# Kernel tuning notes

Hardware: AMD Instinct MI355X
Metric: run time of the kernel (lower is better)

Reference implementation:

```python
import jax, jax.numpy as jnp
import numpy as np

ENT_TYPE_SIZE = 9
INNER_DIM = 64
NEG_INF = 1e12


def _rope_interleaved(x, cos_pos, sin_pos):
    # x: (B, S, H, D); rotate interleaved pairs: (x0,x1)->(x0*c - x1*s, x1*c + x0*s)
    x2 = jnp.stack([-x[..., 1::2], x[..., ::2]], axis=-1).reshape(x.shape)
    return x * cos_pos + x2 * sin_pos


def setup_inputs() -> dict:
    key = jax.random.key(0)
    k1, k2 = jax.random.split(key)
    B, S, H = 16, 512, 768
    out_dim = ENT_TYPE_SIZE * INNER_DIM * 2  # 1152
    last_hidden_state = jax.random.normal(k1, (B, S, H), dtype=jnp.float32)
    attention_mask = jnp.ones((B, S), dtype=jnp.float32)
    W_dense = jax.random.normal(k2, (H, out_dim), dtype=jnp.float32) * (1.0 / np.sqrt(H))
    b_dense = jnp.zeros((out_dim,), dtype=jnp.float32)
    return {
        "last_hidden_state": last_hidden_state,
        "attention_mask": attention_mask,
        "W_dense": W_dense,
        "b_dense": b_dense,
    }


def reference(last_hidden_state, attention_mask, W_dense, b_dense):
    B, S, H = last_hidden_state.shape
    ent, inner = ENT_TYPE_SIZE, INNER_DIM

    # dense projection then split into per-entity-type q/k vectors
    proj = last_hidden_state @ W_dense + b_dense            # (B, S, ent*2*inner)
    proj = proj.reshape(B, S, ent, 2 * inner)
    qw, kw = proj[..., :inner], proj[..., inner:]           # (B, S, ent, inner)

    # inline RoPE, interleaved sin/cos layout per sinusoidal_position_embedding
    pos = jnp.arange(S, dtype=jnp.float32)[:, None]         # (S, 1)
    idx = jnp.arange(inner // 2, dtype=jnp.float32)
    freqs = pos * jnp.power(10000.0, -2.0 * idx / inner)    # (S, inner/2)
    cos_pos = jnp.repeat(jnp.cos(freqs), 2, axis=-1)[None, :, None, :]  # (1,S,1,inner)
    sin_pos = jnp.repeat(jnp.sin(freqs), 2, axis=-1)[None, :, None, :]
    qw = _rope_interleaved(qw, cos_pos, sin_pos)
    kw = _rope_interleaved(kw, cos_pos, sin_pos)

    # pairwise span scores
    logits = jnp.einsum('bmhd,bnhd->bhmn', qw, kw)          # (B, ent, S, S)

    # padding mask on key positions (canonical GlobalPointer masking)
    pad = attention_mask[:, None, None, :]                  # (B,1,1,S)
    logits = logits * pad - (1.0 - pad) * NEG_INF

    # strict lower triangle masked out (only spans with start <= end)
    tril = jnp.tril(jnp.ones((S, S), dtype=logits.dtype), -1)
    logits = logits - tril * NEG_INF

    return logits / (inner ** 0.5)
```

## Files before the change

kernel.cpp:

```cpp
#include <hip/hip_runtime.h>
#include <hip/hip_bf16.h>
#include <cstdint>

typedef __bf16 bf8 __attribute__((ext_vector_type(8)));
typedef __bf16 bf4 __attribute__((ext_vector_type(4)));
typedef float  f4  __attribute__((ext_vector_type(4)));

typedef const void __attribute__((address_space(1)))* as1_cvp;
typedef void       __attribute__((address_space(3)))* as3_vp;

#define NEG_INF_F 1000000000000.0f

__device__ __forceinline__ void lds_load16(const __bf16* g, __bf16* l) {
    __builtin_amdgcn_global_load_lds((as1_cvp)g, (as3_vp)l, 16, 0, 0);
}

__device__ __forceinline__ void gemm_tile_core(
    const __bf16* __restrict__ Atile, const __bf16* __restrict__ Btile,
    int lda, int ldb, int Ktot,
    __bf16* sA, __bf16* sB, f4 acc[4][4])
{
    const int t    = threadIdx.x;
    const int wave = t >> 6;
    const int lane = t & 63;
    const int quad = lane >> 4;
    const int m16  = lane & 15;
    const int wm   = (wave >> 1) * 64;
    const int wn   = (wave & 1) * 64;

    for (int k0 = 0; k0 < Ktot; k0 += 32) {
        __syncthreads();
#pragma unroll
        for (int i = 0; i < 2; ++i) {
            const int f   = i * 256 + t;
            const int row = f >> 2;
            const int ch  = (f & 3) * 8;
            lds_load16(Atile + (size_t)row * lda + k0 + ch,
                       sA + (i * 256 + wave * 64) * 8);
            lds_load16(Btile + (size_t)row * ldb + k0 + ch,
                       sB + (i * 256 + wave * 64) * 8);
        }
        __syncthreads();

        bf8 af[4], bfr[4];
#pragma unroll
        for (int mi = 0; mi < 4; ++mi)
            af[mi] = *(const bf8*)(sA + (wm + mi * 16 + m16) * 32 + quad * 8);
#pragma unroll
        for (int ni = 0; ni < 4; ++ni)
            bfr[ni] = *(const bf8*)(sB + (wn + ni * 16 + m16) * 32 + quad * 8);
#pragma unroll
        for (int mi = 0; mi < 4; ++mi)
#pragma unroll
            for (int ni = 0; ni < 4; ++ni)
                acc[mi][ni] = __builtin_amdgcn_mfma_f32_16x16x32_bf16(
                    af[mi], bfr[ni], acc[mi][ni], 0, 0, 0);
    }
}

__global__ __launch_bounds__(256) void cast_a_kernel(
    const float* __restrict__ in, __bf16* __restrict__ out, int n4)
{
    int idx = blockIdx.x * 256 + threadIdx.x;
    if (idx < n4) {
        const float4 v = reinterpret_cast<const float4*>(in)[idx];
        bf4 o = { (__bf16)v.x, (__bf16)v.y, (__bf16)v.z, (__bf16)v.w };
        reinterpret_cast<bf4*>(out)[idx] = o;
    }
}

__global__ __launch_bounds__(256) void transpose_w_kernel(
    const float* __restrict__ W, __bf16* __restrict__ Wt)
{
    __shared__ __bf16 tile[32][33];
    const int n0 = blockIdx.x * 32;
    const int k0 = blockIdx.y * 32;
    const int tx = threadIdx.x & 31;
    const int ty = threadIdx.x >> 5;
#pragma unroll
    for (int r = 0; r < 32; r += 8)
        tile[ty + r][tx] = (__bf16)W[(size_t)(k0 + ty + r) * 1152 + n0 + tx];
    __syncthreads();
#pragma unroll
    for (int r = 0; r < 32; r += 8)
        Wt[(size_t)(n0 + ty + r) * 768 + k0 + tx] = tile[tx][ty + r];
}

__global__ __launch_bounds__(256) void proj_rope_kernel(
    const __bf16* __restrict__ A,
    const __bf16* __restrict__ Wt,
    const float*  __restrict__ bias,
    __bf16* __restrict__ qbuf, __bf16* __restrict__ kbuf)
{
    __shared__ __bf16 sA[128 * 32];
    __shared__ __bf16 sB[128 * 32];
    f4 acc[4][4] = {};

    const int rowTile = blockIdx.y * 128;
    const int colTile = blockIdx.x * 128;
    gemm_tile_core(A + (size_t)rowTile * 768, Wt + (size_t)colTile * 768,
                   768, 768, 768, sA, sB, acc);

    const int t = threadIdx.x, wave = t >> 6, lane = t & 63;
    const int quad = lane >> 4, m16 = lane & 15;
    const int wm = (wave >> 1) * 64, wn = (wave & 1) * 64;

#pragma unroll
    for (int ni = 0; ni < 4; ++ni) {
        const int gc = colTile + wn + ni * 16 + m16;
        const float bv = bias[gc];
        const int e  = gc >> 7;
        const int d  = gc & 63;
        const int qk = (gc >> 6) & 1;
        const float theta = exp2f((float)(d >> 1) * -0.4152410118609203f);
        const float sgn = (d & 1) ? 1.0f : -1.0f;
        __bf16* dst = qk ? kbuf : qbuf;
#pragma unroll
        for (int mi = 0; mi < 4; ++mi) {
#pragma unroll
            for (int r = 0; r < 4; ++r) {
                const int gm = rowTile + wm + mi * 16 + quad * 4 + r;
                const int bb = gm >> 9;
                const int s  = gm & 511;
                float v = acc[mi][ni][r] + bv;
                float p = __shfl_xor(v, 1);
                float sn, cs;
                __sincosf((float)s * theta, &sn, &cs);
                float o = v * cs + sgn * p * sn;
                dst[(size_t)(((bb * 9 + e) * 512 + s)) * 64 + d] = (__bf16)o;
            }
        }
    }
}

__global__ __launch_bounds__(256, 3) void logits_kernel(
    const __bf16* __restrict__ qbuf, const __bf16* __restrict__ kbuf,
    const float* __restrict__ amask, float* __restrict__ out)
{
    __shared__ __bf16 sQ[2 * 128 * 32];
    __shared__ __bf16 sK[2][2 * 128 * 32];

    const int t    = threadIdx.x;
    const int wave = t >> 6;
    const int lane = t & 63;
    const int quad = lane >> 4;
    const int m16  = lane & 15;
    const int wm   = (wave >> 1) * 64;
    const int wn   = (wave & 1) * 64;

    const int be = blockIdx.y;
    const int b  = be / 9;
    const int rowTile = blockIdx.x * 128;
    const __bf16* Qg = qbuf + (size_t)be * 512 * 64 + (size_t)rowTile * 64;
    const __bf16* Kg = kbuf + (size_t)be * 512 * 64;

#pragma unroll
    for (int i = 0; i < 4; ++i) {
        const int l = i * 256 + t;
        const int p = l >> 9;
        const int r = (l >> 2) & 127;
        const int j = l & 3;
        const int g = r * 8 + p * 4 + j;
        lds_load16(Qg + g * 8, sQ + (i * 256 + wave * 64) * 8);
        lds_load16(Kg + g * 8, sK[0] + (i * 256 + wave * 64) * 8);
    }
    __syncthreads();

    for (int c = 0; c < 4; ++c) {
        if (c < 3) {
            const __bf16* Kc = Kg + (size_t)(c + 1) * 128 * 64;
            __bf16* dstb = sK[(c + 1) & 1];
#pragma unroll
            for (int i = 0; i < 4; ++i) {
                const int l = i * 256 + t;
                const int p = l >> 9;
                const int r = (l >> 2) & 127;
                const int j = l & 3;
                const int g = r * 8 + p * 4 + j;
                lds_load16(Kc + g * 8, dstb + (i * 256 + wave * 64) * 8);
            }
        }

        const __bf16* sKc = sK[c & 1];
        f4 acc[4][4] = {};
#pragma unroll
        for (int kp = 0; kp < 2; ++kp) {
            bf8 af[4], bfr[4];
#pragma unroll
            for (int mi = 0; mi < 4; ++mi)
                af[mi] = *(const bf8*)(sQ + kp * 4096 + (wm + mi * 16 + m16) * 32 + quad * 8);
#pragma unroll
            for (int ni = 0; ni < 4; ++ni)
                bfr[ni] = *(const bf8*)(sKc + kp * 4096 + (wn + ni * 16 + m16) * 32 + quad * 8);
#pragma unroll
            for (int mi = 0; mi < 4; ++mi)
#pragma unroll
                for (int ni = 0; ni < 4; ++ni)
                    acc[mi][ni] = __builtin_amdgcn_mfma_f32_16x16x32_bf16(
                        af[mi], bfr[ni], acc[mi][ni], 0, 0, 0);
        }

        const int colTile = c * 128;
#pragma unroll
        for (int ni = 0; ni < 4; ++ni) {
            const int n = colTile + wn + ni * 16 + m16;
            const float pad    = amask[b * 512 + n];
            const float padoff = (1.0f - pad) * NEG_INF_F;
#pragma unroll
            for (int mi = 0; mi < 4; ++mi) {
#pragma unroll
                for (int r = 0; r < 4; ++r) {
                    const int m = rowTile + wm + mi * 16 + quad * 4 + r;
                    float v = acc[mi][ni][r] * pad - padoff;
                    if (n < m) v -= NEG_INF_F;
                    out[((size_t)(be * 512 + m) << 9) + n] = v * 0.125f;
                }
            }
        }
        __syncthreads();
    }
}

extern "C" void kernel_launch(void* const* d_in, const int* in_sizes, int n_in,
                              void* d_out, int out_size, void* d_ws, size_t ws_size,
                              hipStream_t stream) {
    const float* lhs   = (const float*)d_in[0];
    const float* amask = (const float*)d_in[1];
    const float* W     = (const float*)d_in[2];
    const float* bias  = (const float*)d_in[3];
    float* out = (float*)d_out;

    char* ws = (char*)d_ws;
    __bf16* Abf = (__bf16*)ws;
    __bf16* Wt  = (__bf16*)(ws + 12582912);
    __bf16* qb  = (__bf16*)(ws + 14352384);
    __bf16* kb  = (__bf16*)(ws + 23789568);

    cast_a_kernel<<<6144, 256, 0, stream>>>(lhs, Abf, 1572864);
    transpose_w_kernel<<<dim3(36, 24), 256, 0, stream>>>(W, Wt);
    proj_rope_kernel<<<dim3(9, 64), 256, 0, stream>>>(Abf, Wt, bias, qb, kb);
    logits_kernel<<<dim3(4, 144), 256, 0, stream>>>(qb, kb, amask, out);
}
```

Before: 227.6 us.

## Drop LDS staging in logits kernel; swap MFMA operands for float4 stores

The logits kernel now loads Q fragments straight from global memory into registers once per wave, and loads K fragments per 64-column chunk directly, removing LDS staging and all block barriers. MFMA operands are swapped so each lane holds four consecutive output columns, which allows float4 vectorized stores of the output and a float4 mask load. Each wave now covers 64 rows by 256 columns in four chunks instead of sharing 128x128 tiles. The output write stream dominates this kernel, so wider stores should help, at the cost of redundant global K reads across waves and no prefetch overlap.

```diff
diff --git a/kernel.cpp b/kernel.cpp
--- a/kernel.cpp
+++ b/kernel.cpp
@@ -137,87 +137,76 @@
     const __bf16* __restrict__ qbuf, const __bf16* __restrict__ kbuf,
     const float* __restrict__ amask, float* __restrict__ out)
 {
-    __shared__ __bf16 sQ[2 * 128 * 32];
-    __shared__ __bf16 sK[2][2 * 128 * 32];
-
     const int t    = threadIdx.x;
     const int wave = t >> 6;
     const int lane = t & 63;
     const int quad = lane >> 4;
     const int m16  = lane & 15;
     const int wm   = (wave >> 1) * 64;
-    const int wn   = (wave & 1) * 64;
+    const int ncol = (wave & 1) * 256;
 
     const int be = blockIdx.y;
     const int b  = be / 9;
     const int rowTile = blockIdx.x * 128;
-    const __bf16* Qg = qbuf + (size_t)be * 512 * 64 + (size_t)rowTile * 64;
+
+    const __bf16* Qg = qbuf + (size_t)be * 512 * 64 + (size_t)(rowTile + wm) * 64;
     const __bf16* Kg = kbuf + (size_t)be * 512 * 64;
 
-#pragma unroll
-    for (int i = 0; i < 4; ++i) {
-        const int l = i * 256 + t;
-        const int p = l >> 9;
-        const int r = (l >> 2) & 127;
-        const int j = l & 3;
-        const int g = r * 8 + p * 4 + j;
-        lds_load16(Qg + g * 8, sQ + (i * 256 + wave * 64) * 8);
-        lds_load16(Kg + g * 8, sK[0] + (i * 256 + wave * 64) * 8);
-    }
-    __syncthreads();
-
+    bf8 af[2][4];
+#pragma unroll
+    for (int kp = 0; kp < 2; ++kp)
+#pragma unroll
+        for (int mi = 0; mi < 4; ++mi)
+            af[kp][mi] = *reinterpret_cast<const bf8*>(
+                Qg + (mi * 16 + m16) * 64 + kp * 32 + quad * 8);
+
+    const float* amr  = amask + b * 512;
+    float*       outw = out + ((size_t)(be * 512 + rowTile + wm) << 9);
+
+#pragma unroll 1
     for (int c = 0; c < 4; ++c) {
-        if (c < 3) {
-            const __bf16* Kc = Kg + (size_t)(c + 1) * 128 * 64;
-            __bf16* dstb = sK[(c + 1) & 1];
-#pragma unroll
-            for (int i = 0; i < 4; ++i) {
-                const int l = i * 256 + t;
-                const int p = l >> 9;
-                const int r = (l >> 2) & 127;
-                const int j = l & 3;
-                const int g = r * 8 + p * 4 + j;
-                lds_load16(Kc + g * 8, dstb + (i * 256 + wave * 64) * 8);
+        const int n0 = ncol + c * 64;
+        const __bf16* Kc = Kg + (size_t)n0 * 64;
+
+        bf8 bfr[2][4];
+#pragma unroll
+        for (int kp = 0; kp < 2; ++kp)
+#pragma unroll
+            for (int ni = 0; ni < 4; ++ni)
+                bfr[kp][ni] = *reinterpret_cast<const bf8*>(
+                    Kc + (ni * 16 + m16) * 64 + kp * 32 + quad * 8);
+
+        f4 acc[4][4] = {};
+#pragma unroll
+        for (int kp = 0; kp < 2; ++kp)
+#pragma unroll
+            for (int mi = 0; mi < 4; ++mi)
+#pragma unroll
+                for (int ni = 0; ni < 4; ++ni)
+                    acc[mi][ni] = __builtin_amdgcn_mfma_f32_16x16x32_bf16(
+                        bfr[kp][ni], af[kp][mi], acc[mi][ni], 0, 0, 0);
+
+#pragma unroll
+        for (int ni = 0; ni < 4; ++ni) {
+            const int nq = n0 + ni * 16 + quad * 4;
+            const float4 pv = *reinterpret_cast<const float4*>(amr + nq);
+#pragma unroll
+            for (int mi = 0; mi < 4; ++mi) {
+                const int m = rowTile + wm + mi * 16 + m16;
+                const f4 a = acc[mi][ni];
+                float4 res;
+                float* rp = &res.x;
+                const float pp[4] = { pv.x, pv.y, pv.z, pv.w };
+#pragma unroll
+                for (int r = 0; r < 4; ++r) {
+                    float v = a[r] * pp[r] - (1.0f - pp[r]) * NEG_INF_F;
+                    if (nq + r < m) v -= NEG_INF_F;
+                    rp[r] = v * 0.125f;
+                }
+                *reinterpret_cast<float4*>(
+                    outw + (((size_t)(mi * 16 + m16)) << 9) + nq) = res;
             }
         }
-
-        const __bf16* sKc = sK[c & 1];
-        f4 acc[4][4] = {};
-#pragma unroll
-        for (int kp = 0; kp < 2; ++kp) {
-            bf8 af[4], bfr[4];
-#pragma unroll
-            for (int mi = 0; mi < 4; ++mi)
-                af[mi] = *(const bf8*)(sQ + kp * 4096 + (wm + mi * 16 + m16) * 32 + quad * 8);
-#pragma unroll
-            for (int ni = 0; ni < 4; ++ni)
-                bfr[ni] = *(const bf8*)(sKc + kp * 4096 + (wn + ni * 16 + m16) * 32 + quad * 8);
-#pragma unroll
-            for (int mi = 0; mi < 4; ++mi)
-#pragma unroll
-                for (int ni = 0; ni < 4; ++ni)
-                    acc[mi][ni] = __builtin_amdgcn_mfma_f32_16x16x32_bf16(
-                        af[mi], bfr[ni], acc[mi][ni], 0, 0, 0);
-        }
-
-        const int colTile = c * 128;
-#pragma unroll
-        for (int ni = 0; ni < 4; ++ni) {
-            const int n = colTile + wn + ni * 16 + m16;
-            const float pad    = amask[b * 512 + n];
-            const float padoff = (1.0f - pad) * NEG_INF_F;
-#pragma unroll
-            for (int mi = 0; mi < 4; ++mi) {
-#pragma unroll
-                for (int r = 0; r < 4; ++r) {
-                    const int m = rowTile + wm + mi * 16 + quad * 4 + r;
-                    float v = acc[mi][ni][r] * pad - padoff;
-                    if (n < m) v -= NEG_INF_F;
-                    out[((size_t)(be * 512 + m) << 9) + n] = v * 0.125f;
-                }
-            }
-        }
-        __syncthreads();
     }
 }
 
```

Result: slower. 237.1 us (+4.2%).
